# Performance work log

Hardware: AMD Instinct MI355X
Metric: run time of the kernel (lower is better)

The kernel has to match this reference:

```python
import jax, jax.numpy as jnp
import numpy as np

B, DH, P, V, NP, K = 8, 1024, 64, 50257, 256, 8
SKEW = P * (P - 1) // 2


def setup_inputs() -> dict:
    key = jax.random.key(0)
    ks = jax.random.split(key, 24)
    f = jax.random.normal
    h_t = f(ks[0], (B, DH), jnp.float32)
    R = f(ks[1], (B, P, P), jnp.float32)
    A_t = 0.05 * (R - jnp.swapaxes(R, -1, -2))  # skew-symmetric
    B_t = f(ks[2], (B, NP, P), jnp.float32)
    E = f(ks[3], (V, P), jnp.float32)
    e_mask = f(ks[4], (B, P), jnp.float32)
    M = f(ks[5], (B, P, P), jnp.float32)
    G_tilde = jnp.eye(P) + 0.01 * jnp.einsum('bij,bkj->bik', M, M)  # SPD metric
    z0 = f(ks[6], (B, P), jnp.float32)
    s = lambda k_, sh: f(k_, sh, jnp.float32) * 0.02
    params = dict(
        WQ_w=s(ks[7], (DH, P)), WQ_b=jnp.zeros((P,)),
        WK_w=s(ks[8], (P, P)), WK_b=jnp.zeros((P,)),
        WV_w=s(ks[9], (P, P)), WV_b=jnp.zeros((P,)),
        WC_w=s(ks[10], (P, P)), WC_b=jnp.zeros((P,)),
        WO_w=s(ks[11], (DH, V)),
        WG_w=s(ks[12], (P, P)), WG_b=jnp.zeros((P,)),
        wgamma_w=s(ks[13], (DH + P + SKEW, 1)), wgamma_b=jnp.zeros((1,)),
        wmu_w=s(ks[14], (DH + P + 2, 1)), wmu_b=jnp.zeros((1,)),
        gdown_w=s(ks[15], (SKEW, P)),
        Sigma_inv=jnp.ones((P,)) * 0.1,
        hlie_w=s(ks[16], (DH, P)), hlie_b=jnp.zeros((P,)),
    )
    return dict(h_t=h_t, A_t=A_t, B_t=B_t, E=E, e_mask=e_mask,
                G_tilde=G_tilde, z0=z0, **params)


def _sq_riem(x, Y, G):
    # x: (B,p), Y: (B,n,p), G: (B,p,p) -> (B,n)
    d = Y - x[:, None, :]
    return jnp.einsum('bnp,bpq,bnq->bn', d, G, d)


def reference(h_t, A_t, B_t, E, e_mask, G_tilde, z0,
              WQ_w, WQ_b, WK_w, WK_b, WV_w, WV_b, WC_w, WC_b, WO_w,
              WG_w, WG_b, wgamma_w, wgamma_b, wmu_w, wmu_b,
              gdown_w, Sigma_inv, hlie_w, hlie_b):
    p = A_t.shape[-1]
    scale = 1.0 / jnp.sqrt(jnp.asarray(p, h_t.dtype))
    I = jnp.eye(p, dtype=A_t.dtype)
    Q_t = jnp.linalg.solve(I - A_t, jnp.broadcast_to(I + A_t, A_t.shape))  # Cayley map (B,p,p)
    q_t = h_t @ WQ_w + WQ_b                      # (B,p)
    B_rot = jnp.einsum('bnp,bpq->bnq', B_t, Q_t)  # (B,n,p)
    K_t = B_rot @ WK_w + WK_b
    V_t = B_rot @ WV_w + WV_b
    h_lie = h_t @ hlie_w + hlie_b                 # (B,p)
    omega = -0.5 * _sq_riem(h_lie, B_rot, G_tilde)  # (B,n)
    scores = jnp.einsum('bp,bnp->bn', q_t, K_t) * scale + omega
    alpha = jax.nn.softmax(scores, axis=-1)
    c_t = jnp.einsum('bn,bnp->bp', alpha, V_t)
    iu0, iu1 = jnp.triu_indices(p, k=1)
    g_t = A_t[:, iu0, iu1]                        # (B, skew_dim)
    E_gen = E @ WG_w + WG_b                       # (V,p)
    g_proj = g_t @ gdown_w                        # (B,p)
    diff = E_gen[None, :, :] - g_proj[:, None, :]  # (B,V,p)
    kappa = -jnp.sum(diff * diff * Sigma_inv, axis=-1)  # (B,V)
    base_logits = h_t @ WO_w                      # (B,V)
    c_rot = jnp.einsum('bp,bpq->bq', c_t @ WC_w + WC_b, Q_t)
    group_logits = c_rot @ E.T * scale + kappa
    gamma = jax.nn.sigmoid(jnp.concatenate([h_t, c_t, g_t], -1) @ wgamma_w + wgamma_b)
    logits = base_logits + gamma * group_logits
    pi = jax.nn.softmax(logits, axis=-1)
    topv, topi = jax.lax.top_k(pi, K)
    topp = topv / jnp.sum(topv, -1, keepdims=True)
    E_g = E[topi]                                 # (B,k,p) gather
    E_G = jnp.einsum('bkp,bpq->bkq', E_g, Q_t)
    E_exp = jnp.einsum('bk,bkp->bp', topp, E_G)
    H = -jnp.sum(pi * jnp.log(pi + 1e-12), -1, keepdims=True)
    rho = _sq_riem(h_lie, E_exp[:, None, :], G_tilde)  # (B,1)
    mu = jax.nn.sigmoid(jnp.concatenate([h_t, c_t, H, rho], -1) @ wmu_w + wmu_b)
    m_next = mu * e_mask + (1.0 - mu) * E_exp
    outer = m_next[:, :, None] * e_mask[:, None, :]
    A_next = A_t + 0.1 * (outer - jnp.swapaxes(outer, 1, 2))
    return logits, m_next, A_next
```

## Files before the change

### kernel.cpp

```cpp
#include <hip/hip_runtime.h>
#include <math.h>

#define NV    50257
#define OUT_M 402056
#define OUT_A 402568
#define SCALE 0.125f

#define WS_Q      0
#define WS_HTR    32768
#define WS_S      40960
#define WS_TV     45056
#define WS_C0     45120
#define WS_HLIE   47144
#define WS_GH     48176
#define WS_WB     83008
#define WS_CONSTB 83520
#define WS_GAMMA  83528
#define WS_CT     83536
#define WS_P6     84048

__global__ __launch_bounds__(256) void k_batch(
    const float* __restrict__ h_t, const float* __restrict__ A_t,
    const float* __restrict__ G_t, const float* __restrict__ B_t,
    const float* __restrict__ WG_w, const float* __restrict__ WG_b,
    const float* __restrict__ Sigma_inv,
    const float* __restrict__ WQ_w, const float* __restrict__ WQ_b,
    const float* __restrict__ WK_w,
    const float* __restrict__ WV_w, const float* __restrict__ WV_b,
    const float* __restrict__ WC_w, const float* __restrict__ WC_b,
    const float* __restrict__ wgamma_w, const float* __restrict__ wgamma_b,
    const float* __restrict__ gdown_w,
    const float* __restrict__ hlie_w, const float* __restrict__ hlie_b,
    float* __restrict__ ws)
{
    __shared__ float Ash[64][65];
    __shared__ float Gsh[64][65];
    __shared__ float Bq[64][65];
    __shared__ float hsh[1024];
    __shared__ float piv[2][132];
    __shared__ float fr[2][64];
    __shared__ float dsh[64];
    __shared__ float part[4][64], partb[4][64];
    __shared__ float qt[64], hl[64], qkv[64], ghl[64], v0[64], w1sh[64];
    __shared__ float sc[256], rr[256];
    __shared__ float cBr[64], cB[64], ct[64], cw[64], crot[64], gp[64], uv[64];
    __shared__ float gsh[2016];
    __shared__ float red4[4];
    __shared__ float scal[1];

    const int tid = threadIdx.x;
    const int blk = blockIdx.x;

    if (blk == 8) {
        const int a   = tid & 63;
        const int cb8 = __builtin_amdgcn_readfirstlane(tid >> 6);
        float* sig = hsh;
        float* bg  = hsh + 64;
        if (tid < 64) { sig[tid] = Sigma_inv[tid]; bg[tid] = WG_b[tid]; }
        __syncthreads();
        for (int idx = tid; idx < 4096; idx += 256) {
            int r = idx >> 6, c = idx & 63;
            float wv = WG_w[idx];
            Gsh[r][c] = wv;
            Ash[r][c] = wv * sig[c];
        }
        __syncthreads();
        float t8[16];
        #pragma unroll
        for (int j = 0; j < 16; ++j) t8[j] = 0.0f;
        for (int p = 0; p < 64; ++p) {
            float wv = Ash[a][p];
            #pragma unroll
            for (int jj = 0; jj < 16; ++jj) t8[jj] = fmaf(wv, Gsh[cb8*16 + jj][p], t8[jj]);
        }
        #pragma unroll
        for (int jj = 0; jj < 16; ++jj)
            ws[WS_S + a*64 + cb8*16 + jj] = t8[jj];
        if (cb8 == 0) {
            float s = 0.0f;
            for (int p = 0; p < 64; ++p) s += Ash[a][p] * bg[p];
            ws[WS_TV + a] = 2.0f * s;
        }
        if (tid == 0) {
            float c0 = 0.0f;
            for (int p = 0; p < 64; ++p) c0 += sig[p] * bg[p] * bg[p];
            ws[WS_C0] = c0;
        }
        return;
    }

    const int b  = blk;
    const int i  = tid & 63;
    const int cb = __builtin_amdgcn_readfirstlane(tid >> 6);
    const int col0 = cb * 16;

    for (int idx = tid; idx < 4096; idx += 256) {
        int r = idx >> 6, c = idx & 63;
        Ash[r][c] = A_t[b*4096 + idx];
        Gsh[r][c] = G_t[b*4096 + idx];
    }
    for (int k = tid; k < 1024; k += 256) {
        float hv = h_t[b*1024 + k];
        hsh[k] = hv;
        ws[WS_HTR + k*8 + b] = hv;
    }
    __syncthreads();

    for (int idx = tid; idx < 4096; idx += 256) {
        int i2 = idx >> 6, j2 = idx & 63;
        if (j2 > i2) {
            int s = i2*63 - ((i2*(i2-1)) >> 1) + (j2 - i2 - 1);
            gsh[s] = Ash[i2][j2];
        }
    }

    float w[32];
    if (cb < 2) {
        #pragma unroll
        for (int jj = 0; jj < 32; ++jj) {
            int j = cb*32 + jj;
            w[jj] = (i == j ? 1.0f : 0.0f) - Ash[i][j];
        }
    } else {
        #pragma unroll
        for (int jj = 0; jj < 32; ++jj) {
            int j = (cb - 2)*32 + jj;
            w[jj] = (i == j ? 1.0f : 0.0f) + Ash[i][j];
        }
    }
    __syncthreads();

    #pragma unroll
    for (int k = 0; k < 64; ++k) {
        const int kb  = k >> 5;
        const int sel = k & 1;
        if (cb == kb) fr[sel][i] = w[k & 31];
        if (i == k) {
            #pragma unroll
            for (int q4 = 0; q4 < 8; ++q4)
                *(float4*)&piv[sel][cb*32 + q4*4] =
                    make_float4(w[q4*4], w[q4*4+1], w[q4*4+2], w[q4*4+3]);
        }
        __syncthreads();
        float pk = piv[sel][k];
        float f = (i == k) ? 0.0f : (fr[sel][i] / pk);
        #pragma unroll
        for (int jj = 0; jj < 32; ++jj)
            w[jj] -= f * piv[sel][cb*32 + jj];
    }

    if (cb == (i >> 5)) dsh[i] = w[i & 31];
    __syncthreads();
    if (cb >= 2) {
        float dinv = 1.0f / dsh[i];
        #pragma unroll
        for (int jj = 0; jj < 32; ++jj)
            Ash[i][(cb - 2)*32 + jj] = w[jj] * dinv;
    }
    __syncthreads();
    for (int idx = tid; idx < 4096; idx += 256)
        ws[WS_Q + b*4096 + idx] = Ash[idx >> 6][idx & 63];

    {
        float aq0 = 0, aq1 = 0, ah0 = 0, ah1 = 0, ag0 = 0, ag1 = 0;
        #pragma unroll 8
        for (int kk = 0; kk < 256; kk += 2) {
            int k = cb*256 + kk;
            float hv0 = hsh[k], hv1 = hsh[k + 1];
            aq0 = fmaf(hv0, WQ_w[k*64 + i], aq0);
            aq1 = fmaf(hv1, WQ_w[(k+1)*64 + i], aq1);
            ah0 = fmaf(hv0, hlie_w[k*64 + i], ah0);
            ah1 = fmaf(hv1, hlie_w[(k+1)*64 + i], ah1);
            ag0 = fmaf(hv0, wgamma_w[k], ag0);
            ag1 = fmaf(hv1, wgamma_w[k+1], ag1);
        }
        part[cb][i] = aq0 + aq1;
        partb[cb][i] = ah0 + ah1;
        if (i == 0) red4[cb] = ag0 + ag1;
    }
    __syncthreads();
    if (tid < 64) {
        qt[tid] = part[0][tid]+part[1][tid]+part[2][tid]+part[3][tid] + WQ_b[tid];
        hl[tid] = partb[0][tid]+partb[1][tid]+partb[2][tid]+partb[3][tid] + hlie_b[tid];
    }
    if (tid == 0) scal[0] = red4[0]+red4[1]+red4[2]+red4[3];
    __syncthreads();
    {
        float acc = 0;
        #pragma unroll
        for (int jj = 0; jj < 16; ++jj)
            acc = fmaf(WK_w[i*64 + col0 + jj], qt[col0 + jj], acc);
        part[cb][i] = acc;
    }
    __syncthreads();
    if (tid < 64) qkv[tid] = part[0][tid]+part[1][tid]+part[2][tid]+part[3][tid];
    __syncthreads();
    {
        float acc = 0;
        #pragma unroll
        for (int jj = 0; jj < 16; ++jj)
            acc = fmaf(Gsh[i][col0 + jj], hl[col0 + jj], acc);
        part[cb][i] = acc;
    }
    __syncthreads();
    if (tid < 64) {
        ghl[tid] = part[0][tid]+part[1][tid]+part[2][tid]+part[3][tid];
        v0[tid]  = SCALE*qkv[tid] + ghl[tid];
    }
    __syncthreads();
    {
        float acc = 0;
        #pragma unroll
        for (int jj = 0; jj < 16; ++jj)
            acc = fmaf(Ash[i][col0 + jj], v0[col0 + jj], acc);
        part[cb][i] = acc;
    }
    __syncthreads();
    if (tid < 64) {
        w1sh[tid] = part[0][tid]+part[1][tid]+part[2][tid]+part[3][tid];
        ws[WS_HLIE + b*64 + tid] = hl[tid];
    }
    float tt[16];
    #pragma unroll
    for (int j = 0; j < 16; ++j) tt[j] = 0;
    for (int r = 0; r < 64; ++r) {
        float qv = Ash[i][r];
        #pragma unroll
        for (int j = 0; j < 16; ++j) tt[j] = fmaf(qv, Gsh[r][col0 + j], tt[j]);
    }
    __syncthreads();
    #pragma unroll
    for (int j = 0; j < 16; ++j) Gsh[i][col0 + j] = tt[j];
    __syncthreads();
    float w2r[16];
    #pragma unroll
    for (int j = 0; j < 16; ++j) w2r[j] = 0;
    for (int q = 0; q < 64; ++q) {
        float tv = Gsh[i][q];
        #pragma unroll
        for (int j = 0; j < 16; ++j) w2r[j] = fmaf(tv, Ash[col0 + j][q], w2r[j]);
    }
    __syncthreads();
    #pragma unroll
    for (int j = 0; j < 16; ++j) Gsh[col0 + j][i] = w2r[j];
    __syncthreads();

    for (int q4 = 0; q4 < 4; ++q4) {
        for (int idx = tid; idx < 4096; idx += 256) {
            int r = idx >> 6, c = idx & 63;
            Bq[r][c] = B_t[b*16384 + (q4*64 + r)*64 + c];
        }
        __syncthreads();
        float ts[16];
        #pragma unroll
        for (int j = 0; j < 16; ++j) ts[j] = 0;
        for (int p = 0; p < 64; ++p) {
            float bv = Bq[i][p];
            #pragma unroll
            for (int j = 0; j < 16; ++j) ts[j] = fmaf(bv, Gsh[p][col0 + j], ts[j]);
        }
        float ps = 0;
        #pragma unroll
        for (int j = 0; j < 16; ++j)
            ps += (w1sh[col0+j] - 0.5f*ts[j]) * Bq[i][col0+j];
        part[cb][i] = ps;
        __syncthreads();
        if (tid < 64)
            sc[q4*64 + tid] = part[0][tid]+part[1][tid]+part[2][tid]+part[3][tid];
        __syncthreads();
    }

    float svv = sc[tid];
    rr[tid] = svv; __syncthreads();
    for (int off = 128; off > 0; off >>= 1) { if (tid < off) rr[tid] = fmaxf(rr[tid], rr[tid+off]); __syncthreads(); }
    float smax = rr[0]; __syncthreads();
    float e = expf(svv - smax);
    rr[tid] = e; __syncthreads();
    for (int off = 128; off > 0; off >>= 1) { if (tid < off) rr[tid] += rr[tid+off]; __syncthreads(); }
    float den = rr[0]; __syncthreads();
    sc[tid] = e / den;
    __syncthreads();
    {
        float acc = 0;
        for (int nn = 0; nn < 64; ++nn) {
            int n = cb*64 + nn;
            acc = fmaf(sc[n], B_t[b*16384 + n*64 + i], acc);
        }
        part[cb][i] = acc;
    }
    __syncthreads();
    if (tid < 64) cBr[tid] = part[0][tid]+part[1][tid]+part[2][tid]+part[3][tid];
    __syncthreads();
    {
        float acc = 0;
        #pragma unroll
        for (int pp = 0; pp < 16; ++pp) { int p = col0+pp; acc = fmaf(cBr[p], Ash[p][i], acc); }
        part[cb][i] = acc;
    }
    __syncthreads();
    if (tid < 64) cB[tid] = part[0][tid]+part[1][tid]+part[2][tid]+part[3][tid];
    __syncthreads();
    {
        float acc = 0;
        #pragma unroll
        for (int pp = 0; pp < 16; ++pp) { int p = col0+pp; acc = fmaf(cB[p], WV_w[p*64+i], acc); }
        part[cb][i] = acc;
    }
    __syncthreads();
    if (tid < 64) {
        float v = part[0][tid]+part[1][tid]+part[2][tid]+part[3][tid] + WV_b[tid];
        ct[tid] = v; ws[WS_CT + b*64 + tid] = v;
    }
    __syncthreads();
    {
        float acc = 0;
        #pragma unroll
        for (int pp = 0; pp < 16; ++pp) { int p = col0+pp; acc = fmaf(ct[p], WC_w[p*64+i], acc); }
        part[cb][i] = acc;
    }
    __syncthreads();
    if (tid < 64) cw[tid] = part[0][tid]+part[1][tid]+part[2][tid]+part[3][tid] + WC_b[tid];
    __syncthreads();
    {
        float acc = 0;
        #pragma unroll
        for (int pp = 0; pp < 16; ++pp) { int p = col0+pp; acc = fmaf(cw[p], Ash[p][i], acc); }
        part[cb][i] = acc;
    }
    __syncthreads();
    if (tid < 64) crot[tid] = part[0][tid]+part[1][tid]+part[2][tid]+part[3][tid];
    __syncthreads();
    {
        float accp0 = 0, accp1 = 0, accg0 = 0, accg1 = 0;
        #pragma unroll 4
        for (int ss = 0; ss < 504; ss += 2) {
            int s = cb*504 + ss;
            float av0 = gsh[s], av1 = gsh[s + 1];
            accp0 = fmaf(av0, gdown_w[s*64 + i], accp0);
            accp1 = fmaf(av1, gdown_w[(s+1)*64 + i], accp1);
            accg0 = fmaf(av0, wgamma_w[1088 + s], accg0);
            accg1 = fmaf(av1, wgamma_w[1089 + s], accg1);
        }
        part[cb][i] = accp0 + accp1;
        if (i == 0) rr[cb] = accg0 + accg1;
    }
    if (tid < 64) rr[64 + tid] = ct[tid] * wgamma_w[1024 + tid];
    __syncthreads();
    if (tid < 64) {
        float g = part[0][tid]+part[1][tid]+part[2][tid]+part[3][tid];
        gp[tid] = g; uv[tid] = 2.0f * Sigma_inv[tid] * g;
    }
    if (tid == 0) {
        float gc = 0; for (int j = 0; j < 64; ++j) gc += rr[64 + j];
        float z = scal[0] + gc + rr[0]+rr[1]+rr[2]+rr[3] + wgamma_b[0];
        ws[WS_GAMMA + b] = 1.0f / (1.0f + expf(-z));
    }
    __syncthreads();
    {
        float acc = 0;
        #pragma unroll
        for (int pp = 0; pp < 16; ++pp) { int p = col0+pp; acc = fmaf(WG_w[i*64+p], uv[p], acc); }
        part[cb][i] = acc;
    }
    if (tid < 64) rr[tid] = WG_b[tid]*uv[tid] - gp[tid]*gp[tid]*Sigma_inv[tid];
    __syncthreads();
    if (tid < 64)
        ws[WS_WB + b*64 + tid] = SCALE*crot[tid]
            + part[0][tid]+part[1][tid]+part[2][tid]+part[3][tid];
    if (tid == 0) { float s = 0; for (int j = 0; j < 64; ++j) s += rr[j]; ws[WS_CONSTB + b] = s; }
}

#define KU 16
__global__ __launch_bounds__(256) void k5_logits(
    const float* __restrict__ E, const float* __restrict__ WO_w,
    const float* __restrict__ ws, float* __restrict__ out)
{
    __shared__ float smem[11600];
    const int tid = threadIdx.x;
    const int q   = tid >> 6;
    const int vt  = tid & 63;
    const int vb  = blockIdx.x * 64;
    const int v   = vb + vt;
    const bool vok = v < NV;
    const int vv = vok ? v : NV - 1;

    float* Esh  = smem;
    float* Ssh  = smem + 4224;
    float* tvsh = smem + 8448;
    float* wbsh = smem + 8512;
    float* gmsh = smem + 9024;
    float* cbsh = smem + 9032;
    float* svsh = smem + 9040;
    float* gdsh = smem + 9296;
    float* accsh= smem + 9872;
    float* hsh  = smem;

    for (int idx = tid; idx < 1024; idx += 256) {
        int r = idx >> 4, c4 = (idx & 15) * 4;
        int vr = vb + r; if (vr >= NV) vr = NV - 1;
        float4 e4 = *(const float4*)(E + (size_t)vr * 64 + c4);
        float* dst = Esh + r*66 + c4;
        dst[0] = e4.x; dst[1] = e4.y; dst[2] = e4.z; dst[3] = e4.w;
    }
    for (int idx = tid; idx < 4096; idx += 256) Ssh[idx] = ws[WS_S + idx];
    for (int idx = tid; idx < 512; idx += 256) wbsh[idx] = ws[WS_WB + idx];
    if (tid < 64) tvsh[tid] = ws[WS_TV + tid];
    if (tid < 8) { gmsh[tid] = ws[WS_GAMMA + tid]; cbsh[tid] = ws[WS_CONSTB + tid]; }
    __syncthreads();
    {
        const float* er = Esh + vt*66;
        float sv = (q == 0) ? ws[WS_C0] : 0.0f;
        {
            float t[16];
            #pragma unroll
            for (int j = 0; j < 16; ++j) t[j] = 0.0f;
            for (int p = 0; p < 64; ++p) {
                float ep = er[p];
                #pragma unroll
                for (int j = 0; j < 16; ++j)
                    t[j] = fmaf(ep, Ssh[p*64 + q*16 + j], t[j]);
            }
            #pragma unroll
            for (int j = 0; j < 16; ++j)
                sv += (t[j] + tvsh[q*16 + j]) * er[q*16 + j];
        }
        svsh[q*64 + vt] = sv;
        const float* w0 = wbsh + (2*q    )*64;
        const float* w1 = wbsh + (2*q + 1)*64;
        float g0 = 0, g1 = 0;
        #pragma unroll 8
        for (int p = 0; p < 64; ++p) {
            float ep = er[p];
            g0 = fmaf(ep, w0[p], g0); g1 = fmaf(ep, w1[p], g1);
        }
        gdsh[vt*9 + 2*q]     = g0;
        gdsh[vt*9 + 2*q + 1] = g1;
    }
    __syncthreads();
    for (int idx = tid; idx < 2048; idx += 256)
        *(float4*)(hsh + idx*4) = *(const float4*)(ws + WS_HTR + idx*4);
    __syncthreads();
    float acc[8];
    #pragma unroll
    for (int bb = 0; bb < 8; ++bb) acc[bb] = 0.0f;
    {
        const float* wo = WO_w + (size_t)(q * 256) * NV + vv;
        const float* hb = hsh + q*256*8;
        for (int k0 = 0; k0 < 256; k0 += KU) {
            float wr[KU];
            #pragma unroll
            for (int u = 0; u < KU; ++u) wr[u] = wo[(size_t)(k0 + u) * NV];
            #pragma unroll
            for (int u = 0; u < KU; ++u) {
                const float* hp = hb + (k0 + u)*8;
                #pragma unroll
                for (int bb = 0; bb < 8; ++bb) acc[bb] = fmaf(hp[bb], wr[u], acc[bb]);
            }
        }
    }
    if (q) {
        float* ar = accsh + (q-1)*576 + vt*9;
        #pragma unroll
        for (int bb = 0; bb < 8; ++bb) ar[bb] = acc[bb];
    }
    __syncthreads();
    if (q == 0 && vok) {
        float svt = svsh[vt] + svsh[64+vt] + svsh[128+vt] + svsh[192+vt];
        const float* gr = gdsh + vt*9;
        #pragma unroll
        for (int bb = 0; bb < 8; ++bb) {
            float a = acc[bb] + accsh[vt*9+bb] + accsh[576+vt*9+bb] + accsh[1152+vt*9+bb];
            float gl = gr[bb] + cbsh[bb] - svt;
            out[bb*NV + v] = fmaf(gmsh[bb], gl, a);
        }
    }
}

#define NQ 12565
__global__ __launch_bounds__(256) void k6a_scan(
    const float* __restrict__ outl, float* __restrict__ ws)
{
    __shared__ float mvw[4][8];
    __shared__ int   miw[4][8];
    __shared__ float t8v[8];
    __shared__ int   t8i[8];
    __shared__ float redv[4], sred[4];
    const int b = blockIdx.x >> 2, qq = blockIdx.x & 3;
    const int tid = threadIdx.x, lane = tid & 63, wvi = tid >> 6;
    const int v0 = qq * NQ;
    const int v1 = (v0 + NQ < NV) ? (v0 + NQ) : NV;
    const float* lg = outl + b*NV;

    float lv[8]; int li[8];
    #pragma unroll
    for (int u = 0; u < 8; ++u) { lv[u] = -INFINITY; li[u] = 0x7fffffff; }
    float mt = -INFINITY, s1 = 0.0f, s2 = 0.0f;
    for (int v = v0 + tid; v < v1; v += 256) {
        float x = lg[v];
        if (x > mt) {
            float r = expf(mt - x);
            s1 *= r; s2 *= r; mt = x;
        }
        float ee = expf(x - mt);
        s1 += ee; s2 += x * ee;
        if (x > lv[7]) {
            float cv = x; int ci = v;
            #pragma unroll
            for (int u = 0; u < 8; ++u) {
                if (cv > lv[u]) {
                    float tv = lv[u]; lv[u] = cv; cv = tv;
                    int   ti = li[u]; li[u] = ci; ci = ti;
                }
            }
        }
    }
    float wv8[8]; int wi8[8];
    #pragma unroll
    for (int it = 0; it < 8; ++it) {
        float bv = lv[0]; int bi = li[0];
        #pragma unroll
        for (int off = 32; off > 0; off >>= 1) {
            float ov = __shfl_xor(bv, off);
            int   oi = __shfl_xor(bi, off);
            if (ov > bv || (ov == bv && oi < bi)) { bv = ov; bi = oi; }
        }
        wv8[it] = bv; wi8[it] = bi;
        if (lv[0] == bv && li[0] == bi) {
            lv[0]=lv[1]; lv[1]=lv[2]; lv[2]=lv[3]; lv[3]=lv[4];
            lv[4]=lv[5]; lv[5]=lv[6]; lv[6]=lv[7]; lv[7]=-INFINITY;
            li[0]=li[1]; li[1]=li[2]; li[2]=li[3]; li[3]=li[4];
            li[4]=li[5]; li[5]=li[6]; li[6]=li[7]; li[7]=0x7fffffff;
        }
    }
    if (lane == 0) {
        #pragma unroll
        for (int u = 0; u < 8; ++u) { mvw[wvi][u] = wv8[u]; miw[wvi][u] = wi8[u]; }
    }
    __syncthreads();
    if (tid == 0) {
        int pA = 0, pB = 0, pC = 0, pD = 0;
        for (int it = 0; it < 8; ++it) {
            float vA = mvw[0][pA], vB = mvw[1][pB], vC = mvw[2][pC], vD = mvw[3][pD];
            int   iA = miw[0][pA], iB = miw[1][pB], iC = miw[2][pC], iD = miw[3][pD];
            float best = vA; int bi = iA; int w = 0;
            if (vB > best || (vB == best && iB < bi)) { best = vB; bi = iB; w = 1; }
            if (vC > best || (vC == best && iC < bi)) { best = vC; bi = iC; w = 2; }
            if (vD > best || (vD == best && iD < bi)) { best = vD; bi = iD; w = 3; }
            t8v[it] = best; t8i[it] = bi;
            if (w == 0) ++pA; else if (w == 1) ++pB; else if (w == 2) ++pC; else ++pD;
        }
    }
    __syncthreads();
    float Mp = t8v[0];
    {
        float r = expf(mt - Mp);
        s1 *= r; s2 *= r;
    }
    #pragma unroll
    for (int off = 32; off > 0; off >>= 1) {
        s1 += __shfl_xor(s1, off);
        s2 += __shfl_xor(s2, off);
    }
    if (lane == 0) { redv[wvi] = s1; sred[wvi] = s2; }
    __syncthreads();
    if (tid == 0) {
        int base = WS_P6 + (b*4 + qq)*20;
        #pragma unroll
        for (int u = 0; u < 8; ++u) { ws[base + u] = t8v[u]; ((int*)ws)[base + 8 + u] = t8i[u]; }
        ws[base + 16] = Mp;
        ws[base + 17] = redv[0]+redv[1]+redv[2]+redv[3];
        ws[base + 18] = sred[0]+sred[1]+sred[2]+sred[3];
    }
}

__global__ __launch_bounds__(256) void k6b_final(
    const float* __restrict__ h_t, const float* __restrict__ A_t,
    const float* __restrict__ E, const float* __restrict__ e_mask,
    const float* __restrict__ G_t,
    const float* __restrict__ wmu_w, const float* __restrict__ wmu_b,
    const float* __restrict__ ws, float* __restrict__ out)
{
    __shared__ float mv[32];
    __shared__ int   mi[32];
    __shared__ float t8v[8];
    __shared__ int   t8i[8];
    __shared__ float toppsh[8];
    __shared__ float redv[256];
    __shared__ float uvec[64], eexp[64], msh[64], emsh[64];
    __shared__ float scal[4];
    const int b = blockIdx.x, tid = threadIdx.x;

    if (tid < 32) {
        int base = WS_P6 + (b*4 + (tid >> 3))*20;
        mv[tid] = ws[base + (tid & 7)];
        mi[tid] = ((const int*)ws)[base + 8 + (tid & 7)];
    }
    __syncthreads();
    if (tid == 0) {
        unsigned used = 0;
        for (int it = 0; it < 8; ++it) {
            float best = -INFINITY; int bi = 0x7fffffff, bs = 0;
            for (int c = 0; c < 32; ++c) {
                if (used & (1u << c)) continue;
                float x = mv[c];
                if (x > best || (x == best && mi[c] < bi)) { best = x; bi = mi[c]; bs = c; }
            }
            used |= 1u << bs; t8v[it] = best; t8i[it] = bi;
        }
        float M = t8v[0];
        float s1 = 0, s2 = 0;
        for (int q = 0; q < 4; ++q) {
            int base = WS_P6 + (b*4 + q)*20;
            float sc_ = expf(ws[base + 16] - M);
            s1 += ws[base + 17] * sc_; s2 += ws[base + 18] * sc_;
        }
        scal[0] = M + logf(s1) - s2 / s1;
        float ts = 0, tv_[8];
        #pragma unroll
        for (int u = 0; u < 8; ++u) { tv_[u] = expf(t8v[u] - M); ts += tv_[u]; }
        #pragma unroll
        for (int u = 0; u < 8; ++u) toppsh[u] = tv_[u] / ts;
    }
    __syncthreads();
    if (tid < 64) {
        float u_ = 0;
        #pragma unroll
        for (int j = 0; j < 8; ++j) u_ += toppsh[j] * E[t8i[j]*64 + tid];
        uvec[tid] = u_;
    }
    __syncthreads();
    if (tid < 64) {
        const float* Qb = ws + WS_Q + b*4096;
        float a = 0;
        for (int p = 0; p < 64; ++p) a += uvec[p] * Qb[p*64 + tid];
        eexp[tid] = a;
    }
    __syncthreads();
    {
        const float* Gb = G_t + b*4096;
        const float* HL = ws + WS_HLIE + b*64;
        float a = 0;
        #pragma unroll 4
        for (int t2 = 0; t2 < 16; ++t2) {
            int idx = tid*16 + t2;
            int p = idx >> 6, q = idx & 63;
            a += (eexp[p] - HL[p]) * Gb[idx] * (eexp[q] - HL[q]);
        }
        redv[tid] = a;
    }
    __syncthreads();
    for (int off = 128; off > 0; off >>= 1) {
        if (tid < off) redv[tid] += redv[tid + off];
        __syncthreads();
    }
    if (tid == 0) scal[1] = redv[0];
    __syncthreads();
    float pm = 0;
    for (int k = tid; k < 1024; k += 256) pm += h_t[b*1024 + k] * wmu_w[k];
    if (tid < 64) pm += ws[WS_CT + b*64 + tid] * wmu_w[1024 + tid];
    redv[tid] = pm;
    __syncthreads();
    for (int off = 128; off > 0; off >>= 1) {
        if (tid < off) redv[tid] += redv[tid + off];
        __syncthreads();
    }
    if (tid == 0) {
        float z = redv[0] + scal[0]*wmu_w[1088] + scal[1]*wmu_w[1089] + wmu_b[0];
        scal[2] = 1.0f / (1.0f + expf(-z));
    }
    __syncthreads();
    if (tid < 64) {
        float mu = scal[2];
        float em = e_mask[b*64 + tid];
        float m = mu*em + (1.0f - mu)*eexp[tid];
        out[OUT_M + b*64 + tid] = m;
        msh[tid] = m; emsh[tid] = em;
    }
    __syncthreads();
    for (int idx = tid; idx < 4096; idx += 256) {
        int i = idx >> 6, j = idx & 63;
        out[OUT_A + b*4096 + idx] = A_t[b*4096 + idx]
            + 0.1f*(msh[i]*emsh[j] - msh[j]*emsh[i]);
    }
}

extern "C" void kernel_launch(void* const* d_in, const int* in_sizes, int n_in,
                              void* d_out, int out_size, void* d_ws, size_t ws_size,
                              hipStream_t stream)
{
    const float* h_t      = (const float*)d_in[0];
    const float* A_t      = (const float*)d_in[1];
    const float* B_t      = (const float*)d_in[2];
    const float* E        = (const float*)d_in[3];
    const float* e_mask   = (const float*)d_in[4];
    const float* G_t      = (const float*)d_in[5];
    const float* WQ_w     = (const float*)d_in[7];
    const float* WQ_b     = (const float*)d_in[8];
    const float* WK_w     = (const float*)d_in[9];
    const float* WV_w     = (const float*)d_in[11];
    const float* WV_b     = (const float*)d_in[12];
    const float* WC_w     = (const float*)d_in[13];
    const float* WC_b     = (const float*)d_in[14];
    const float* WO_w     = (const float*)d_in[15];
    const float* WG_w     = (const float*)d_in[16];
    const float* WG_b     = (const float*)d_in[17];
    const float* wgamma_w = (const float*)d_in[18];
    const float* wgamma_b = (const float*)d_in[19];
    const float* wmu_w    = (const float*)d_in[20];
    const float* wmu_b    = (const float*)d_in[21];
    const float* gdown_w  = (const float*)d_in[22];
    const float* Sigma_inv= (const float*)d_in[23];
    const float* hlie_w   = (const float*)d_in[24];
    const float* hlie_b   = (const float*)d_in[25];
    float* out = (float*)d_out;
    float* ws  = (float*)d_ws;

    k_batch<<<9, 256, 0, stream>>>(h_t, A_t, G_t, B_t, WG_w, WG_b, Sigma_inv,
                                   WQ_w, WQ_b, WK_w, WV_w, WV_b, WC_w, WC_b,
                                   wgamma_w, wgamma_b, gdown_w,
                                   hlie_w, hlie_b, ws);
    k5_logits<<<786, 256, 0, stream>>>(E, WO_w, ws, out);
    k6a_scan<<<32, 256, 0, stream>>>(out, ws);
    k6b_final<<<8, 256, 0, stream>>>(h_t, A_t, E, e_mask, G_t, wmu_w, wmu_b, ws, out);
}
```

Measured before the change: 582.2 us.

## Split serial per-batch kernel into four stages to spread work across more blocks

Replaces the single 9-block per-batch kernel with four kernels. A 57-block prep kernel runs the Cayley solve alongside split-K partial products for h·WQ, h·hlie, gdown and the gamma terms. A chain kernel reduces the partials, a 32-block scores kernel handles the B_t quadratic form, and a mid kernel does the softmax and attention. The aim is to cut the long serial latency of a few blocks doing 1024-long and 2016-long reductions on a GPU with many idle CUs. In exchange it adds three launches and workspace round trips for intermediates.

```diff
diff --git a/kernel.cpp b/kernel.cpp
--- a/kernel.cpp
+++ b/kernel.cpp
@@ -12,44 +12,98 @@
 #define WS_TV     45056
 #define WS_C0     45120
 #define WS_HLIE   47144
+#define WS_W1     47656
 #define WS_GH     48176
+#define WS_WMAT   48192
+#define WS_SC     80960
 #define WS_WB     83008
 #define WS_CONSTB 83520
 #define WS_GAMMA  83528
 #define WS_CT     83536
 #define WS_P6     84048
-
-__global__ __launch_bounds__(256) void k_batch(
+#define WS_PQT    86016
+#define WS_PHL    94208
+#define WS_PGH    102400
+#define WS_PGP    102528
+#define WS_PGG    118912
+
+__global__ __launch_bounds__(256) void kA_prep(
     const float* __restrict__ h_t, const float* __restrict__ A_t,
-    const float* __restrict__ G_t, const float* __restrict__ B_t,
     const float* __restrict__ WG_w, const float* __restrict__ WG_b,
     const float* __restrict__ Sigma_inv,
-    const float* __restrict__ WQ_w, const float* __restrict__ WQ_b,
-    const float* __restrict__ WK_w,
-    const float* __restrict__ WV_w, const float* __restrict__ WV_b,
-    const float* __restrict__ WC_w, const float* __restrict__ WC_b,
-    const float* __restrict__ wgamma_w, const float* __restrict__ wgamma_b,
-    const float* __restrict__ gdown_w,
-    const float* __restrict__ hlie_w, const float* __restrict__ hlie_b,
+    const float* __restrict__ WQ_w, const float* __restrict__ wgamma_w,
+    const float* __restrict__ hlie_w, const float* __restrict__ gdown_w,
     float* __restrict__ ws)
 {
     __shared__ float Ash[64][65];
     __shared__ float Gsh[64][65];
-    __shared__ float Bq[64][65];
     __shared__ float hsh[1024];
     __shared__ float piv[2][132];
     __shared__ float fr[2][64];
     __shared__ float dsh[64];
-    __shared__ float part[4][64], partb[4][64];
-    __shared__ float qt[64], hl[64], qkv[64], ghl[64], v0[64], w1sh[64];
-    __shared__ float sc[256], rr[256];
-    __shared__ float cBr[64], cB[64], ct[64], cw[64], crot[64], gp[64], uv[64];
-    __shared__ float gsh[2016];
-    __shared__ float red4[4];
-    __shared__ float scal[1];
 
     const int tid = threadIdx.x;
     const int blk = blockIdx.x;
+
+    if (blk < 8) {
+        const int b  = blk;
+        const int i  = tid & 63;
+        const int cb = __builtin_amdgcn_readfirstlane(tid >> 6);
+
+        for (int idx = tid; idx < 4096; idx += 256)
+            Ash[idx >> 6][idx & 63] = A_t[b*4096 + idx];
+        for (int k = tid; k < 1024; k += 256)
+            ws[WS_HTR + k*8 + b] = h_t[b*1024 + k];
+        __syncthreads();
+
+        float w[32];
+        if (cb < 2) {
+            #pragma unroll
+            for (int jj = 0; jj < 32; ++jj) {
+                int j = cb*32 + jj;
+                w[jj] = (i == j ? 1.0f : 0.0f) - Ash[i][j];
+            }
+        } else {
+            #pragma unroll
+            for (int jj = 0; jj < 32; ++jj) {
+                int j = (cb - 2)*32 + jj;
+                w[jj] = (i == j ? 1.0f : 0.0f) + Ash[i][j];
+            }
+        }
+        __syncthreads();
+
+        #pragma unroll
+        for (int k = 0; k < 64; ++k) {
+            const int kb  = k >> 5;
+            const int sel = k & 1;
+            if (cb == kb) fr[sel][i] = w[k & 31];
+            if (i == k) {
+                #pragma unroll
+                for (int q4 = 0; q4 < 8; ++q4)
+                    *(float4*)&piv[sel][cb*32 + q4*4] =
+                        make_float4(w[q4*4], w[q4*4+1], w[q4*4+2], w[q4*4+3]);
+            }
+            __syncthreads();
+            float pk = piv[sel][k];
+            float f = (i == k) ? 0.0f : (fr[sel][i] / pk);
+            #pragma unroll
+            for (int jj = 0; jj < 32; ++jj)
+                w[jj] -= f * piv[sel][cb*32 + jj];
+        }
+
+        if (cb == (i >> 5)) dsh[i] = w[i & 31];
+        __syncthreads();
+        if (cb >= 2) {
+            float dinv = 1.0f / dsh[i];
+            #pragma unroll
+            for (int jj = 0; jj < 32; ++jj)
+                Ash[i][(cb - 2)*32 + jj] = w[jj] * dinv;
+        }
+        __syncthreads();
+        for (int idx = tid; idx < 4096; idx += 256)
+            ws[WS_Q + b*4096 + idx] = Ash[idx >> 6][idx & 63];
+        return;
+    }
 
     if (blk == 8) {
         const int a   = tid & 63;
@@ -89,101 +143,134 @@
         return;
     }
 
-    const int b  = blk;
-    const int i  = tid & 63;
+    if (blk < 25) {
+        const int c = blk - 9;
+        const int i = tid & 63;
+        const int w = __builtin_amdgcn_readfirstlane(tid >> 6);
+        for (int idx = tid; idx < 4096; idx += 256) {
+            int r = idx >> 6, col = idx & 63;
+            int krow = c*64 + r;
+            Ash[r][col] = WQ_w[krow*64 + col];
+            Gsh[r][col] = hlie_w[krow*64 + col];
+        }
+        for (int t = tid; t < 512; t += 256) {
+            int b = t >> 6, kk = t & 63;
+            hsh[b*64 + kk] = h_t[b*1024 + c*64 + kk];
+        }
+        if (tid < 64) dsh[tid] = wgamma_w[c*64 + tid];
+        __syncthreads();
+        const int b0 = 2*w, b1 = 2*w + 1;
+        float q0 = 0, q1 = 0, l0 = 0, l1 = 0;
+        #pragma unroll 8
+        for (int kk = 0; kk < 64; ++kk) {
+            float a = Ash[kk][i], g = Gsh[kk][i];
+            float h0 = hsh[b0*64 + kk], h1 = hsh[b1*64 + kk];
+            q0 = fmaf(h0, a, q0); q1 = fmaf(h1, a, q1);
+            l0 = fmaf(h0, g, l0); l1 = fmaf(h1, g, l1);
+        }
+        ws[WS_PQT + (c*8 + b0)*64 + i] = q0;
+        ws[WS_PQT + (c*8 + b1)*64 + i] = q1;
+        ws[WS_PHL + (c*8 + b0)*64 + i] = l0;
+        ws[WS_PHL + (c*8 + b1)*64 + i] = l1;
+        float g0 = hsh[b0*64 + i] * dsh[i];
+        float g1 = hsh[b1*64 + i] * dsh[i];
+        #pragma unroll
+        for (int off = 32; off > 0; off >>= 1) {
+            g0 += __shfl_xor(g0, off);
+            g1 += __shfl_xor(g1, off);
+        }
+        if (i == 0) {
+            ws[WS_PGH + c*8 + b0] = g0;
+            ws[WS_PGH + c*8 + b1] = g1;
+        }
+        return;
+    }
+
+    {
+        const int c = blk - 25;
+        const int i = tid & 63;
+        const int w = __builtin_amdgcn_readfirstlane(tid >> 6);
+        for (int idx = tid; idx < 4032; idx += 256) {
+            int r = idx >> 6, col = idx & 63;
+            Ash[r][col] = gdown_w[(c*63 + r)*64 + col];
+        }
+        for (int t = tid; t < 504; t += 256) {
+            int b = t / 63, sl = t % 63;
+            int s = c*63 + sl;
+            int i2 = 0, f = 0;
+            while (f + (63 - i2) <= s) { f += 63 - i2; ++i2; }
+            int j2 = i2 + 1 + (s - f);
+            hsh[b*63 + sl] = A_t[b*4096 + i2*64 + j2];
+        }
+        if (tid < 63) dsh[tid] = wgamma_w[1088 + c*63 + tid];
+        __syncthreads();
+        const int b0 = 2*w, b1 = 2*w + 1;
+        float a0 = 0, a1 = 0;
+        #pragma unroll 4
+        for (int sl = 0; sl < 63; ++sl) {
+            float gd = Ash[sl][i];
+            a0 = fmaf(hsh[b0*63 + sl], gd, a0);
+            a1 = fmaf(hsh[b1*63 + sl], gd, a1);
+        }
+        ws[WS_PGP + (c*8 + b0)*64 + i] = a0;
+        ws[WS_PGP + (c*8 + b1)*64 + i] = a1;
+        float g0 = (i < 63) ? hsh[b0*63 + i] * dsh[i] : 0.0f;
+        float g1 = (i < 63) ? hsh[b1*63 + i] * dsh[i] : 0.0f;
+        #pragma unroll
+        for (int off = 32; off > 0; off >>= 1) {
+            g0 += __shfl_xor(g0, off);
+            g1 += __shfl_xor(g1, off);
+        }
+        if (i == 0) {
+            ws[WS_PGG + c*8 + b0] = g0;
+            ws[WS_PGG + c*8 + b1] = g1;
+        }
+    }
+}
+
+__global__ __launch_bounds__(256) void kB_chain(
+    const float* __restrict__ G_t,
+    const float* __restrict__ WQ_b, const float* __restrict__ WK_w,
+    const float* __restrict__ hlie_b,
+    float* __restrict__ ws)
+{
+    __shared__ float Qsh[64][65], Gsh[64][65];
+    __shared__ float part[4][64], partb[4][64];
+    __shared__ float qt[64], hl[64], qkv[64], v0[64];
+    __shared__ float red16[16];
+
+    const int b = blockIdx.x, tid = threadIdx.x;
+    const int i = tid & 63;
     const int cb = __builtin_amdgcn_readfirstlane(tid >> 6);
     const int col0 = cb * 16;
 
     for (int idx = tid; idx < 4096; idx += 256) {
         int r = idx >> 6, c = idx & 63;
-        Ash[r][c] = A_t[b*4096 + idx];
+        Qsh[r][c] = ws[WS_Q + b*4096 + idx];
         Gsh[r][c] = G_t[b*4096 + idx];
     }
-    for (int k = tid; k < 1024; k += 256) {
-        float hv = h_t[b*1024 + k];
-        hsh[k] = hv;
-        ws[WS_HTR + k*8 + b] = hv;
-    }
-    __syncthreads();
-
-    for (int idx = tid; idx < 4096; idx += 256) {
-        int i2 = idx >> 6, j2 = idx & 63;
-        if (j2 > i2) {
-            int s = i2*63 - ((i2*(i2-1)) >> 1) + (j2 - i2 - 1);
-            gsh[s] = Ash[i2][j2];
-        }
-    }
-
-    float w[32];
-    if (cb < 2) {
-        #pragma unroll
-        for (int jj = 0; jj < 32; ++jj) {
-            int j = cb*32 + jj;
-            w[jj] = (i == j ? 1.0f : 0.0f) - Ash[i][j];
-        }
-    } else {
-        #pragma unroll
-        for (int jj = 0; jj < 32; ++jj) {
-            int j = (cb - 2)*32 + jj;
-            w[jj] = (i == j ? 1.0f : 0.0f) + Ash[i][j];
-        }
-    }
-    __syncthreads();
-
-    #pragma unroll
-    for (int k = 0; k < 64; ++k) {
-        const int kb  = k >> 5;
-        const int sel = k & 1;
-        if (cb == kb) fr[sel][i] = w[k & 31];
-        if (i == k) {
-            #pragma unroll
-            for (int q4 = 0; q4 < 8; ++q4)
-                *(float4*)&piv[sel][cb*32 + q4*4] =
-                    make_float4(w[q4*4], w[q4*4+1], w[q4*4+2], w[q4*4+3]);
-        }
-        __syncthreads();
-        float pk = piv[sel][k];
-        float f = (i == k) ? 0.0f : (fr[sel][i] / pk);
-        #pragma unroll
-        for (int jj = 0; jj < 32; ++jj)
-            w[jj] -= f * piv[sel][cb*32 + jj];
-    }
-
-    if (cb == (i >> 5)) dsh[i] = w[i & 31];
-    __syncthreads();
-    if (cb >= 2) {
-        float dinv = 1.0f / dsh[i];
-        #pragma unroll
-        for (int jj = 0; jj < 32; ++jj)
-            Ash[i][(cb - 2)*32 + jj] = w[jj] * dinv;
-    }
-    __syncthreads();
-    for (int idx = tid; idx < 4096; idx += 256)
-        ws[WS_Q + b*4096 + idx] = Ash[idx >> 6][idx & 63];
-
-    {
-        float aq0 = 0, aq1 = 0, ah0 = 0, ah1 = 0, ag0 = 0, ag1 = 0;
-        #pragma unroll 8
-        for (int kk = 0; kk < 256; kk += 2) {
-            int k = cb*256 + kk;
-            float hv0 = hsh[k], hv1 = hsh[k + 1];
-            aq0 = fmaf(hv0, WQ_w[k*64 + i], aq0);
-            aq1 = fmaf(hv1, WQ_w[(k+1)*64 + i], aq1);
-            ah0 = fmaf(hv0, hlie_w[k*64 + i], ah0);
-            ah1 = fmaf(hv1, hlie_w[(k+1)*64 + i], ah1);
-            ag0 = fmaf(hv0, wgamma_w[k], ag0);
-            ag1 = fmaf(hv1, wgamma_w[k+1], ag1);
-        }
-        part[cb][i] = aq0 + aq1;
-        partb[cb][i] = ah0 + ah1;
-        if (i == 0) red4[cb] = ag0 + ag1;
-    }
+    {
+        float aq = 0, ah = 0;
+        #pragma unroll
+        for (int cc = 0; cc < 4; ++cc) {
+            int c = cb*4 + cc;
+            aq += ws[WS_PQT + (c*8 + b)*64 + i];
+            ah += ws[WS_PHL + (c*8 + b)*64 + i];
+        }
+        part[cb][i] = aq; partb[cb][i] = ah;
+    }
+    if (tid < 16) red16[tid] = ws[WS_PGH + tid*8 + b];
     __syncthreads();
     if (tid < 64) {
         qt[tid] = part[0][tid]+part[1][tid]+part[2][tid]+part[3][tid] + WQ_b[tid];
         hl[tid] = partb[0][tid]+partb[1][tid]+partb[2][tid]+partb[3][tid] + hlie_b[tid];
     }
-    if (tid == 0) scal[0] = red4[0]+red4[1]+red4[2]+red4[3];
+    if (tid == 0) {
+        float s = 0;
+        #pragma unroll
+        for (int j = 0; j < 16; ++j) s += red16[j];
+        ws[WS_GH + b] = s;
+    }
     __syncthreads();
     {
         float acc = 0;
@@ -203,28 +290,26 @@
         part[cb][i] = acc;
     }
     __syncthreads();
+    if (tid < 64)
+        v0[tid] = SCALE*qkv[tid] + part[0][tid]+part[1][tid]+part[2][tid]+part[3][tid];
+    __syncthreads();
+    {
+        float acc = 0;
+        #pragma unroll
+        for (int jj = 0; jj < 16; ++jj)
+            acc = fmaf(Qsh[i][col0 + jj], v0[col0 + jj], acc);
+        part[cb][i] = acc;
+    }
+    __syncthreads();
     if (tid < 64) {
-        ghl[tid] = part[0][tid]+part[1][tid]+part[2][tid]+part[3][tid];
-        v0[tid]  = SCALE*qkv[tid] + ghl[tid];
-    }
-    __syncthreads();
-    {
-        float acc = 0;
-        #pragma unroll
-        for (int jj = 0; jj < 16; ++jj)
-            acc = fmaf(Ash[i][col0 + jj], v0[col0 + jj], acc);
-        part[cb][i] = acc;
-    }
-    __syncthreads();
-    if (tid < 64) {
-        w1sh[tid] = part[0][tid]+part[1][tid]+part[2][tid]+part[3][tid];
+        ws[WS_W1 + b*64 + tid]   = part[0][tid]+part[1][tid]+part[2][tid]+part[3][tid];
         ws[WS_HLIE + b*64 + tid] = hl[tid];
     }
     float tt[16];
     #pragma unroll
     for (int j = 0; j < 16; ++j) tt[j] = 0;
     for (int r = 0; r < 64; ++r) {
-        float qv = Ash[i][r];
+        float qv = Qsh[i][r];
         #pragma unroll
         for (int j = 0; j < 16; ++j) tt[j] = fmaf(qv, Gsh[r][col0 + j], tt[j]);
     }
@@ -238,55 +323,86 @@
     for (int q = 0; q < 64; ++q) {
         float tv = Gsh[i][q];
         #pragma unroll
-        for (int j = 0; j < 16; ++j) w2r[j] = fmaf(tv, Ash[col0 + j][q], w2r[j]);
-    }
-    __syncthreads();
-    #pragma unroll
-    for (int j = 0; j < 16; ++j) Gsh[col0 + j][i] = w2r[j];
-    __syncthreads();
-
-    for (int q4 = 0; q4 < 4; ++q4) {
-        for (int idx = tid; idx < 4096; idx += 256) {
-            int r = idx >> 6, c = idx & 63;
-            Bq[r][c] = B_t[b*16384 + (q4*64 + r)*64 + c];
-        }
-        __syncthreads();
-        float ts[16];
-        #pragma unroll
-        for (int j = 0; j < 16; ++j) ts[j] = 0;
-        for (int p = 0; p < 64; ++p) {
-            float bv = Bq[i][p];
-            #pragma unroll
-            for (int j = 0; j < 16; ++j) ts[j] = fmaf(bv, Gsh[p][col0 + j], ts[j]);
-        }
-        float ps = 0;
-        #pragma unroll
-        for (int j = 0; j < 16; ++j)
-            ps += (w1sh[col0+j] - 0.5f*ts[j]) * Bq[i][col0+j];
-        part[cb][i] = ps;
-        __syncthreads();
-        if (tid < 64)
-            sc[q4*64 + tid] = part[0][tid]+part[1][tid]+part[2][tid]+part[3][tid];
-        __syncthreads();
-    }
-
-    float svv = sc[tid];
-    rr[tid] = svv; __syncthreads();
+        for (int j = 0; j < 16; ++j) w2r[j] = fmaf(tv, Qsh[col0 + j][q], w2r[j]);
+    }
+    #pragma unroll
+    for (int j = 0; j < 16; ++j)
+        ws[WS_WMAT + b*4096 + (col0 + j)*64 + i] = w2r[j];
+}
+
+__global__ __launch_bounds__(256) void kC_scores(
+    const float* __restrict__ B_t, float* __restrict__ ws)
+{
+    __shared__ float Bsh[64][65];
+    __shared__ float Wsh[64][64];
+    __shared__ float w1sh[64];
+    __shared__ float part[4][64];
+    const int b = blockIdx.x >> 2, q4 = blockIdx.x & 3;
+    const int tid = threadIdx.x, lane = tid & 63;
+    const int gu = __builtin_amdgcn_readfirstlane(tid >> 6);
+    const int col0 = gu * 16;
+    for (int idx = tid; idx < 4096; idx += 256) {
+        int r = idx >> 6, c = idx & 63;
+        Bsh[r][c] = B_t[b*16384 + (q4*64 + r)*64 + c];
+        Wsh[r][c] = ws[WS_WMAT + b*4096 + idx];
+    }
+    if (tid < 64) w1sh[tid] = ws[WS_W1 + b*64 + tid];
+    __syncthreads();
+    float t[16];
+    #pragma unroll
+    for (int j = 0; j < 16; ++j) t[j] = 0;
+    for (int p = 0; p < 64; ++p) {
+        float bv = Bsh[lane][p];
+        #pragma unroll
+        for (int j = 0; j < 16; ++j) t[j] = fmaf(bv, Wsh[p][col0 + j], t[j]);
+    }
+    float ps = 0;
+    #pragma unroll
+    for (int j = 0; j < 16; ++j) ps += (w1sh[col0+j] - 0.5f*t[j]) * Bsh[lane][col0+j];
+    part[gu][lane] = ps;
+    __syncthreads();
+    if (tid < 64)
+        ws[WS_SC + b*256 + q4*64 + tid] =
+            part[0][tid]+part[1][tid]+part[2][tid]+part[3][tid];
+}
+
+__global__ __launch_bounds__(256) void kD_mid(
+    const float* __restrict__ B_t,
+    const float* __restrict__ WV_w, const float* __restrict__ WV_b,
+    const float* __restrict__ WC_w, const float* __restrict__ WC_b,
+    const float* __restrict__ WG_w, const float* __restrict__ WG_b,
+    const float* __restrict__ wgamma_w, const float* __restrict__ wgamma_b,
+    const float* __restrict__ Sigma_inv,
+    float* __restrict__ ws)
+{
+    __shared__ float alpha[256], rr[256];
+    __shared__ float part[4][64];
+    __shared__ float cBr[64], cB[64], ct[64], cw[64], crot[64], gp[64], uv[64];
+    __shared__ float red32[32];
+    const int b = blockIdx.x, tid = threadIdx.x, lane = tid & 63;
+    const int gu = __builtin_amdgcn_readfirstlane(tid >> 6);
+    const int col0 = gu * 16;
+    const float* Qb = ws + WS_Q + b*4096;
+
+    float sv = ws[WS_SC + b*256 + tid];
+    rr[tid] = sv;
+    if (tid < 32) red32[tid] = ws[WS_PGG + tid*8 + b];
+    __syncthreads();
     for (int off = 128; off > 0; off >>= 1) { if (tid < off) rr[tid] = fmaxf(rr[tid], rr[tid+off]); __syncthreads(); }
     float smax = rr[0]; __syncthreads();
-    float e = expf(svv - smax);
+    float e = expf(sv - smax);
     rr[tid] = e; __syncthreads();
     for (int off = 128; off > 0; off >>= 1) { if (tid < off) rr[tid] += rr[tid+off]; __syncthreads(); }
     float den = rr[0]; __syncthreads();
-    sc[tid] = e / den;
+    alpha[tid] = e / den;
     __syncthreads();
     {
         float acc = 0;
         for (int nn = 0; nn < 64; ++nn) {
-            int n = cb*64 + nn;
-            acc = fmaf(sc[n], B_t[b*16384 + n*64 + i], acc);
-        }
-        part[cb][i] = acc;
+            int n = gu*64 + nn;
+            acc = fmaf(alpha[n], B_t[b*16384 + n*64 + lane], acc);
+        }
+        part[gu][lane] = acc;
     }
     __syncthreads();
     if (tid < 64) cBr[tid] = part[0][tid]+part[1][tid]+part[2][tid]+part[3][tid];
@@ -294,8 +410,8 @@
     {
         float acc = 0;
         #pragma unroll
-        for (int pp = 0; pp < 16; ++pp) { int p = col0+pp; acc = fmaf(cBr[p], Ash[p][i], acc); }
-        part[cb][i] = acc;
+        for (int pp = 0; pp < 16; ++pp) { int p = col0+pp; acc = fmaf(cBr[p], Qb[p*64+lane], acc); }
+        part[gu][lane] = acc;
     }
     __syncthreads();
     if (tid < 64) cB[tid] = part[0][tid]+part[1][tid]+part[2][tid]+part[3][tid];
@@ -303,8 +419,8 @@
     {
         float acc = 0;
         #pragma unroll
-        for (int pp = 0; pp < 16; ++pp) { int p = col0+pp; acc = fmaf(cB[p], WV_w[p*64+i], acc); }
-        part[cb][i] = acc;
+        for (int pp = 0; pp < 16; ++pp) { int p = col0+pp; acc = fmaf(cB[p], WV_w[p*64+lane], acc); }
+        part[gu][lane] = acc;
     }
     __syncthreads();
     if (tid < 64) {
@@ -315,8 +431,8 @@
     {
         float acc = 0;
         #pragma unroll
-        for (int pp = 0; pp < 16; ++pp) { int p = col0+pp; acc = fmaf(ct[p], WC_w[p*64+i], acc); }
-        part[cb][i] = acc;
+        for (int pp = 0; pp < 16; ++pp) { int p = col0+pp; acc = fmaf(ct[p], WC_w[p*64+lane], acc); }
+        part[gu][lane] = acc;
     }
     __syncthreads();
     if (tid < 64) cw[tid] = part[0][tid]+part[1][tid]+part[2][tid]+part[3][tid] + WC_b[tid];
@@ -324,25 +440,20 @@
     {
         float acc = 0;
         #pragma unroll
-        for (int pp = 0; pp < 16; ++pp) { int p = col0+pp; acc = fmaf(cw[p], Ash[p][i], acc); }
-        part[cb][i] = acc;
+        for (int pp = 0; pp < 16; ++pp) { int p = col0+pp; acc = fmaf(cw[p], Qb[p*64+lane], acc); }
+        part[gu][lane] = acc;
     }
     __syncthreads();
     if (tid < 64) crot[tid] = part[0][tid]+part[1][tid]+part[2][tid]+part[3][tid];
     __syncthreads();
     {
-        float accp0 = 0, accp1 = 0, accg0 = 0, accg1 = 0;
-        #pragma unroll 4
-        for (int ss = 0; ss < 504; ss += 2) {
-            int s = cb*504 + ss;
-            float av0 = gsh[s], av1 = gsh[s + 1];
-            accp0 = fmaf(av0, gdown_w[s*64 + i], accp0);
-            accp1 = fmaf(av1, gdown_w[(s+1)*64 + i], accp1);
-            accg0 = fmaf(av0, wgamma_w[1088 + s], accg0);
-            accg1 = fmaf(av1, wgamma_w[1089 + s], accg1);
-        }
-        part[cb][i] = accp0 + accp1;
-        if (i == 0) rr[cb] = accg0 + accg1;
+        float acc = 0;
+        #pragma unroll
+        for (int cc = 0; cc < 8; ++cc) {
+            int c = gu*8 + cc;
+            acc += ws[WS_PGP + (c*8 + b)*64 + lane];
+        }
+        part[gu][lane] = acc;
     }
     if (tid < 64) rr[64 + tid] = ct[tid] * wgamma_w[1024 + tid];
     __syncthreads();
@@ -351,16 +462,19 @@
         gp[tid] = g; uv[tid] = 2.0f * Sigma_inv[tid] * g;
     }
     if (tid == 0) {
-        float gc = 0; for (int j = 0; j < 64; ++j) gc += rr[64 + j];
-        float z = scal[0] + gc + rr[0]+rr[1]+rr[2]+rr[3] + wgamma_b[0];
+        float gc = 0;
+        for (int j = 0; j < 64; ++j) gc += rr[64 + j];
+        float ga = 0;
+        for (int j = 0; j < 32; ++j) ga += red32[j];
+        float z = ws[WS_GH + b] + gc + ga + wgamma_b[0];
         ws[WS_GAMMA + b] = 1.0f / (1.0f + expf(-z));
     }
     __syncthreads();
     {
         float acc = 0;
         #pragma unroll
-        for (int pp = 0; pp < 16; ++pp) { int p = col0+pp; acc = fmaf(WG_w[i*64+p], uv[p], acc); }
-        part[cb][i] = acc;
+        for (int pp = 0; pp < 16; ++pp) { int p = col0+pp; acc = fmaf(WG_w[lane*64+p], uv[p], acc); }
+        part[gu][lane] = acc;
     }
     if (tid < 64) rr[tid] = WG_b[tid]*uv[tid] - gp[tid]*gp[tid]*Sigma_inv[tid];
     __syncthreads();
@@ -715,10 +829,12 @@
     float* out = (float*)d_out;
     float* ws  = (float*)d_ws;
 
-    k_batch<<<9, 256, 0, stream>>>(h_t, A_t, G_t, B_t, WG_w, WG_b, Sigma_inv,
-                                   WQ_w, WQ_b, WK_w, WV_w, WV_b, WC_w, WC_b,
-                                   wgamma_w, wgamma_b, gdown_w,
-                                   hlie_w, hlie_b, ws);
+    kA_prep<<<57, 256, 0, stream>>>(h_t, A_t, WG_w, WG_b, Sigma_inv,
+                                    WQ_w, wgamma_w, hlie_w, gdown_w, ws);
+    kB_chain<<<8, 256, 0, stream>>>(G_t, WQ_b, WK_w, hlie_b, ws);
+    kC_scores<<<32, 256, 0, stream>>>(B_t, ws);
+    kD_mid<<<8, 256, 0, stream>>>(B_t, WV_w, WV_b, WC_w, WC_b, WG_w, WG_b,
+                                  wgamma_w, wgamma_b, Sigma_inv, ws);
     k5_logits<<<786, 256, 0, stream>>>(E, WO_w, ws, out);
     k6a_scan<<<32, 256, 0, stream>>>(out, ws);
     k6b_final<<<8, 256, 0, stream>>>(h_t, A_t, E, e_mask, G_t, wmu_w, wmu_b, ws, out);
```

Result: faster. 524.5 us (-9.9%).
